# Kernel tuning notes

Measured on AMD Instinct MI355X. Metric: run time of the kernel, lower is better.

Reference implementation:

```python
import jax, jax.numpy as jnp
import numpy as np

N_HEAD = 16
THETA = 10000.0


def _rope_cos_sin(T, head_dim):
    # freqs: (T, head_dim//2), matches torch.polar(ones, outer(t, 1/theta^(2i/d)))
    inv = 1.0 / (THETA ** (jnp.arange(0, head_dim, 2, dtype=jnp.float32) / head_dim))
    freqs = jnp.arange(T, dtype=jnp.float32)[:, None] * inv[None, :]
    # broadcast shape (1, T, 1, head_dim//2) over (B, T, H, head_dim//2)
    return jnp.cos(freqs)[None, :, None, :], jnp.sin(freqs)[None, :, None, :]


def _apply_rope(t, cos, sin):
    # t: (B, T, H, hd); pairs (even, odd) form complex numbers
    B, T, H, hd = t.shape
    tr = t.astype(jnp.float32).reshape(B, T, H, hd // 2, 2)
    re, im = tr[..., 0], tr[..., 1]
    out = jnp.stack([re * cos - im * sin, re * sin + im * cos], axis=-1)
    return out.reshape(B, T, H, hd).astype(t.dtype)


def setup_inputs() -> dict:
    key = jax.random.key(0)
    k1, k2, k3 = jax.random.split(key, 3)
    C = 1024
    x = jax.random.normal(k1, (4, 2048, C), dtype=jnp.float32)
    w_attn = jax.random.normal(k2, (3 * C, C), dtype=jnp.float32) * 0.02
    w_proj = jax.random.normal(k3, (C, C), dtype=jnp.float32) * 0.02
    return {"x": x, "w_attn": w_attn, "w_proj": w_proj}


def reference(x, w_attn, w_proj):
    B, T, C = x.shape
    H = N_HEAD
    hd = C // H
    qkv = x @ w_attn.T  # (B, T, 3C) fused QKV projection
    q, k, v = jnp.split(qkv, 3, axis=-1)
    q = q.reshape(B, T, H, hd)
    k = k.reshape(B, T, H, hd)
    v = v.reshape(B, T, H, hd).transpose(0, 2, 1, 3)  # (B, H, T, hd)
    cos, sin = _rope_cos_sin(T, hd)
    q = _apply_rope(q, cos, sin).transpose(0, 2, 1, 3)  # (B, H, T, hd)
    k = _apply_rope(k, cos, sin).transpose(0, 2, 1, 3)
    scale = 1.0 / jnp.sqrt(jnp.float32(hd))
    scores = jnp.einsum('bhqd,bhkd->bhqk', q, k) * scale
    attn = jax.nn.softmax(scores, axis=-1)
    y = jnp.einsum('bhqk,bhkd->bhqd', attn, v)  # (B, H, T, hd)
    y = y.transpose(0, 2, 1, 3).reshape(B, T, C)
    return y @ w_proj.T
```

## Files before the change

### kernel.cpp

```cpp
#include <hip/hip_runtime.h>
#include <math.h>

#define BATCH 4
#define TSEQ 2048
#define CDIM 1024
#define NHEAD 16
#define HDIM 64
#define M_ROWS (BATCH * TSEQ)

typedef float f32x4 __attribute__((ext_vector_type(4)));
typedef __bf16 bf16x8 __attribute__((ext_vector_type(8)));
typedef unsigned int u32x4 __attribute__((ext_vector_type(4)));

typedef const __attribute__((address_space(1))) void gas_void;
typedef __attribute__((address_space(3))) void las_void;

static __device__ __forceinline__ unsigned short f2bf(float f) {
    unsigned int x = __float_as_uint(f);
    x += 0x7fffu + ((x >> 16) & 1u);
    return (unsigned short)(x >> 16);
}

__global__ void prep_kernel(const float* __restrict__ x, unsigned short* __restrict__ xb,
                            const float* __restrict__ wa, unsigned short* __restrict__ wab,
                            const float* __restrict__ wp, unsigned short* __restrict__ wpb,
                            float* __restrict__ cosT, float* __restrict__ sinT) {
    int blk = blockIdx.x;
    if (blk < 6144) {
        const float* in;
        unsigned short* out;
        int base;
        if (blk < 4096)      { in = x;  out = xb;  base = blk; }
        else if (blk < 5632) { in = wa; out = wab; base = blk - 4096; }
        else                 { in = wp; out = wpb; base = blk - 5632; }
        int i = (base * 256 + threadIdx.x) << 3;
        float4 a = *(const float4*)(in + i);
        float4 b = *(const float4*)(in + i + 4);
        union { unsigned short u[8]; u32x4 v; } pk;
        pk.u[0] = f2bf(a.x); pk.u[1] = f2bf(a.y); pk.u[2] = f2bf(a.z); pk.u[3] = f2bf(a.w);
        pk.u[4] = f2bf(b.x); pk.u[5] = f2bf(b.y); pk.u[6] = f2bf(b.z); pk.u[7] = f2bf(b.w);
        *(u32x4*)(out + i) = pk.v;
    } else {
        int idx = (blk - 6144) * 256 + threadIdx.x;
        int t = idx >> 5;
        int i = idx & 31;
        double inv = pow(10000.0, -((double)(2 * i)) / (double)HDIM);
        double ph = (double)t * inv;
        cosT[idx] = (float)cos(ph);
        sinT[idx] = (float)sin(ph);
    }
}

#define GROW(p) (((p) & 64) + (((p) & 15) << 2) + (((p) >> 4) & 3))
#define GEMM_CORE(A_, B_, K_, bm_, bn_)                                          \
    const int tid = threadIdx.x;                                                 \
    const int w = tid >> 6, lane = tid & 63;                                     \
    const int l15 = lane & 15, quad = lane >> 4;                                 \
    const int wm = w >> 1, wn = w & 1;                                           \
    const int srow = (w << 5) + (lane >> 2);                                     \
    const int kpart = (lane & 3) << 3;                                           \
    const unsigned short* Ag0 = A_ + (size_t)(bm_ + srow) * K_ + kpart;          \
    const unsigned short* Ag1 = A_ + (size_t)(bm_ + srow + 16) * K_ + kpart;     \
    const unsigned short* Bg0 = B_ + (size_t)(bn_ + GROW(srow)) * K_ + kpart;    \
    const unsigned short* Bg1 = B_ + (size_t)(bn_ + GROW(srow + 16)) * K_ + kpart; \
    unsigned short* Al0 = As + srow * 32 + kpart;                                \
    unsigned short* Al1 = As + (srow + 16) * 32 + kpart;                         \
    unsigned short* Bl0 = Bs + srow * 32 + kpart;                                \
    unsigned short* Bl1 = Bs + (srow + 16) * 32 + kpart;                         \
    f32x4 acc[4][4];                                                             \
    _Pragma("unroll")                                                            \
    for (int i = 0; i < 4; ++i)                                                  \
        _Pragma("unroll")                                                        \
        for (int j = 0; j < 4; ++j) acc[i][j] = (f32x4){0.f, 0.f, 0.f, 0.f};     \
    for (int k0 = 0; k0 < K_; k0 += 32) {                                        \
        __builtin_amdgcn_global_load_lds((gas_void*)(Ag0 + k0), (las_void*)Al0, 16, 0, 0); \
        __builtin_amdgcn_global_load_lds((gas_void*)(Ag1 + k0), (las_void*)Al1, 16, 0, 0); \
        __builtin_amdgcn_global_load_lds((gas_void*)(Bg0 + k0), (las_void*)Bl0, 16, 0, 0); \
        __builtin_amdgcn_global_load_lds((gas_void*)(Bg1 + k0), (las_void*)Bl1, 16, 0, 0); \
        __syncthreads();                                                         \
        bf16x8 af[4], bf[4];                                                     \
        _Pragma("unroll")                                                        \
        for (int mi = 0; mi < 4; ++mi)                                           \
            af[mi] = __builtin_bit_cast(bf16x8,                                  \
                *(const u32x4*)(As + ((wm << 6) + (mi << 4) + l15) * 32 + (quad << 3))); \
        _Pragma("unroll")                                                        \
        for (int ni = 0; ni < 4; ++ni)                                           \
            bf[ni] = __builtin_bit_cast(bf16x8,                                  \
                *(const u32x4*)(Bs + ((wn << 6) + (ni << 4) + l15) * 32 + (quad << 3))); \
        _Pragma("unroll")                                                        \
        for (int mi = 0; mi < 4; ++mi)                                           \
            _Pragma("unroll")                                                    \
            for (int ni = 0; ni < 4; ++ni)                                       \
                acc[mi][ni] = __builtin_amdgcn_mfma_f32_16x16x32_bf16(af[mi], bf[ni], acc[mi][ni], 0, 0, 0); \
        __syncthreads();                                                         \
    }

__global__ __launch_bounds__(256) void gemm_qkv_fused(
        const unsigned short* __restrict__ A, const unsigned short* __restrict__ B,
        unsigned short* __restrict__ qb, unsigned short* __restrict__ kb,
        unsigned short* __restrict__ vb,
        const float* __restrict__ cosT, const float* __restrict__ sinT) {
    __shared__ __align__(16) unsigned short As[128 * 32];
    __shared__ __align__(16) unsigned short Bs[128 * 32];
    const int bm = blockIdx.y << 7;
    const int bn = blockIdx.x << 7;
    GEMM_CORE(A, B, CDIM, bm, bn)

    const int nbase = bn + (wn << 6);
    const int mbase = bm + (wm << 6);
    const int b = mbase >> 11;
    const int tt0 = mbase & (TSEQ - 1);
    const int d0 = l15 << 2;
    const int fi = l15 << 1;

    if (nbase < 2 * CDIM) {
        const int isQ = (nbase < CDIM) ? 1 : 0;
        unsigned short* dst = isQ ? qb : kb;
        const float qs = isQ ? 0.18033688f : 1.0f;
        const int h = (nbase & (CDIM - 1)) >> 6;
        unsigned short* hb = dst + (size_t)(b * NHEAD + h) * TSEQ * HDIM;
#pragma unroll
        for (int mi = 0; mi < 4; ++mi) {
#pragma unroll
            for (int r = 0; r < 4; ++r) {
                const int t = tt0 + (mi << 4) + (quad << 2) + r;
                float2 cc = *(const float2*)(cosT + (t << 5) + fi);
                float2 ss = *(const float2*)(sinT + (t << 5) + fi);
                float re0 = acc[mi][0][r], im0 = acc[mi][1][r];
                float re1 = acc[mi][2][r], im1 = acc[mi][3][r];
                union { unsigned short u[4]; uint2 v; } pk;
                pk.u[0] = f2bf((re0 * cc.x - im0 * ss.x) * qs);
                pk.u[1] = f2bf((re0 * ss.x + im0 * cc.x) * qs);
                pk.u[2] = f2bf((re1 * cc.y - im1 * ss.y) * qs);
                pk.u[3] = f2bf((re1 * ss.y + im1 * cc.y) * qs);
                *(uint2*)(hb + (size_t)t * HDIM + d0) = pk.v;
            }
        }
    } else {
        const int h = (nbase - 2 * CDIM) >> 6;
        unsigned short* hb = vb + (size_t)(b * NHEAD + h) * HDIM * TSEQ;
#pragma unroll
        for (int mi = 0; mi < 4; ++mi) {
            const int t0 = tt0 + (mi << 4) + (quad << 2);
#pragma unroll
            for (int ni = 0; ni < 4; ++ni) {
                const int d = d0 + ni;
                union { unsigned short u[4]; uint2 v; } pk;
#pragma unroll
                for (int r = 0; r < 4; ++r) pk.u[r] = f2bf(acc[mi][ni][r]);
                *(uint2*)(hb + (size_t)d * TSEQ + t0) = pk.v;
            }
        }
    }
}

__global__ __launch_bounds__(256) void gemm_proj(
        const unsigned short* __restrict__ A, const unsigned short* __restrict__ B,
        float* __restrict__ C) {
    __shared__ __align__(16) unsigned short As[128 * 32];
    __shared__ __align__(16) unsigned short Bs[128 * 32];
    const int bm = blockIdx.y << 7;
    const int bn = blockIdx.x << 7;
    GEMM_CORE(A, B, CDIM, bm, bn)

#pragma unroll
    for (int mi = 0; mi < 4; ++mi)
#pragma unroll
        for (int r = 0; r < 4; ++r) {
            const int row = bm + (wm << 6) + (mi << 4) + (quad << 2) + r;
            float4 v = make_float4(acc[mi][0][r], acc[mi][1][r], acc[mi][2][r], acc[mi][3][r]);
            *(float4*)(C + (size_t)row * CDIM + bn + (wn << 6) + (l15 << 2)) = v;
        }
}

#define KTILE 64
#define NKT (TSEQ / KTILE)
#define QBLK 256
#define SWZ(row, ch) (((row) << 6) + ((((ch) ^ ((row) & 7))) << 3))
__global__ __launch_bounds__(256, 2) void attn_mfma(
        const unsigned short* __restrict__ qb, const unsigned short* __restrict__ kb,
        const unsigned short* __restrict__ vb, unsigned short* __restrict__ y) {
    const int bh = blockIdx.x;
    const int qt = blockIdx.y;
    const int b = bh >> 4, h = bh & 15;
    const int tid  = threadIdx.x;
    const int w    = tid >> 6;
    const int lane = tid & 63;
    const int l15  = lane & 15;
    const int quad = lane >> 4;

    __shared__ __align__(16) unsigned short Ks[2][KTILE * 64];
    __shared__ __align__(16) unsigned short Vs[2][HDIM * 64];
    __shared__ __align__(16) unsigned short Ps[4][64 * 64];

    const size_t qoff = ((size_t)bh * TSEQ + qt * QBLK + w * 64) * HDIM;
    bf16x8 aq[4][2];
#pragma unroll
    for (int mt = 0; mt < 4; ++mt)
#pragma unroll
        for (int kc2 = 0; kc2 < 2; ++kc2) {
            u32x4 v = *(const u32x4*)(qb + qoff + (size_t)(mt * 16 + l15) * HDIM + kc2 * 32 + quad * 8);
            aq[mt][kc2] = __builtin_bit_cast(bf16x8, v);
        }

    f32x4 o[4][4];
    float l_r[4][4];
#pragma unroll
    for (int mt = 0; mt < 4; ++mt)
#pragma unroll
        for (int nc = 0; nc < 4; ++nc) o[mt][nc] = (f32x4){0.f, 0.f, 0.f, 0.f};
#pragma unroll
    for (int mt = 0; mt < 4; ++mt)
#pragma unroll
        for (int r = 0; r < 4; ++r) l_r[mt][r] = 0.f;

    const unsigned short* kbase = kb + (size_t)bh * TSEQ * HDIM;
    const unsigned short* vbase = vb + (size_t)bh * HDIM * TSEQ;

    const int sr = tid >> 3;
    const int sp = (tid & 7) << 3;
    const int pp0 = ((sr & 3) << 4) + (sr >> 2);
    const int st0 = SWZ(pp0, tid & 7);
    const int st1 = SWZ(pp0 + 8, tid & 7);

    u32x4 kr[2], vr[2];
#pragma unroll
    for (int l = 0; l < 2; ++l) {
        int idx = sr + (l << 5);
        kr[l] = *(const u32x4*)(kbase + (size_t)idx * HDIM + sp);
        vr[l] = *(const u32x4*)(vbase + (size_t)idx * TSEQ + sp);
    }
    *(u32x4*)&Ks[0][st0] = kr[0];
    *(u32x4*)&Ks[0][st1] = kr[1];
    *(u32x4*)&Vs[0][st0] = vr[0];
    *(u32x4*)&Vs[0][st1] = vr[1];
#pragma unroll
    for (int l = 0; l < 2; ++l) {
        int idx = sr + (l << 5);
        kr[l] = *(const u32x4*)(kbase + (size_t)(KTILE + idx) * HDIM + sp);
        vr[l] = *(const u32x4*)(vbase + (size_t)idx * TSEQ + KTILE + sp);
    }

    for (int kt = 0; kt < NKT; ++kt) {
        const int cur = kt & 1;
        __syncthreads();

        f32x4 s[4][4];
        __builtin_amdgcn_s_setprio(1);
#pragma unroll
        for (int nc = 0; nc < 4; ++nc) {
            const int rowK = nc * 16 + l15;
            u32x4 k0 = *(const u32x4*)&Ks[cur][SWZ(rowK, quad)];
            u32x4 k1 = *(const u32x4*)&Ks[cur][SWZ(rowK, quad ^ 4)];
            bf16x8 bk0 = __builtin_bit_cast(bf16x8, k0);
            bf16x8 bk1 = __builtin_bit_cast(bf16x8, k1);
#pragma unroll
            for (int mt = 0; mt < 4; ++mt) {
                f32x4 a2 = (f32x4){0.f, 0.f, 0.f, 0.f};
                a2 = __builtin_amdgcn_mfma_f32_16x16x32_bf16(aq[mt][0], bk0, a2, 0, 0, 0);
                a2 = __builtin_amdgcn_mfma_f32_16x16x32_bf16(aq[mt][1], bk1, a2, 0, 0, 0);
                s[mt][nc] = a2;
            }
        }
        __builtin_amdgcn_s_setprio(0);

        if (kt + 1 < NKT) {
            const int nxt = cur ^ 1;
            *(u32x4*)&Ks[nxt][st0] = kr[0];
            *(u32x4*)&Ks[nxt][st1] = kr[1];
            *(u32x4*)&Vs[nxt][st0] = vr[0];
            *(u32x4*)&Vs[nxt][st1] = vr[1];
            if (kt + 2 < NKT) {
                int base = (kt + 2) * KTILE;
#pragma unroll
                for (int l = 0; l < 2; ++l) {
                    int idx = sr + (l << 5);
                    kr[l] = *(const u32x4*)(kbase + (size_t)(base + idx) * HDIM + sp);
                    vr[l] = *(const u32x4*)(vbase + (size_t)idx * TSEQ + base + sp);
                }
            }
        }

#pragma unroll
        for (int mt = 0; mt < 4; ++mt)
#pragma unroll
            for (int r = 0; r < 4; ++r) {
                float p0 = __builtin_amdgcn_exp2f(s[mt][0][r]);
                float p1 = __builtin_amdgcn_exp2f(s[mt][1][r]);
                float p2 = __builtin_amdgcn_exp2f(s[mt][2][r]);
                float p3 = __builtin_amdgcn_exp2f(s[mt][3][r]);
                l_r[mt][r] += (p0 + p1) + (p2 + p3);
                uint2 pk;
                pk.x = __builtin_amdgcn_perm(__float_as_uint(p1), __float_as_uint(p0), 0x07060302u);
                pk.y = __builtin_amdgcn_perm(__float_as_uint(p3), __float_as_uint(p2), 0x07060302u);
                const int rowP = mt * 16 + quad * 4 + r;
                *(uint2*)&Ps[w][SWZ(rowP, l15 >> 1) + ((l15 & 1) << 2)] = pk;
            }
        __threadfence_block();

        bf16x8 ap[4][2];
#pragma unroll
        for (int mt = 0; mt < 4; ++mt)
#pragma unroll
            for (int kc2 = 0; kc2 < 2; ++kc2) {
                const int rowP = mt * 16 + l15;
                u32x4 v = *(const u32x4*)&Ps[w][SWZ(rowP, kc2 * 4 + quad)];
                ap[mt][kc2] = __builtin_bit_cast(bf16x8, v);
            }
        __builtin_amdgcn_s_setprio(1);
#pragma unroll
        for (int nc = 0; nc < 4; ++nc) {
            const int rowV = nc * 16 + l15;
            u32x4 v0 = *(const u32x4*)&Vs[cur][SWZ(rowV, quad)];
            u32x4 v1 = *(const u32x4*)&Vs[cur][SWZ(rowV, quad ^ 4)];
            bf16x8 bv0 = __builtin_bit_cast(bf16x8, v0);
            bf16x8 bv1 = __builtin_bit_cast(bf16x8, v1);
#pragma unroll
            for (int mt = 0; mt < 4; ++mt) {
                o[mt][nc] = __builtin_amdgcn_mfma_f32_16x16x32_bf16(ap[mt][0], bv0, o[mt][nc], 0, 0, 0);
                o[mt][nc] = __builtin_amdgcn_mfma_f32_16x16x32_bf16(ap[mt][1], bv1, o[mt][nc], 0, 0, 0);
            }
        }
        __builtin_amdgcn_s_setprio(0);
    }

#pragma unroll
    for (int off = 1; off < 16; off <<= 1)
#pragma unroll
        for (int mt = 0; mt < 4; ++mt)
#pragma unroll
            for (int r = 0; r < 4; ++r)
                l_r[mt][r] += __shfl_xor(l_r[mt][r], off, 64);

#pragma unroll
    for (int mt = 0; mt < 4; ++mt)
#pragma unroll
        for (int r = 0; r < 4; ++r) {
            float inv_l = 1.f / l_r[mt][r];
            int t = qt * QBLK + w * 64 + mt * 16 + quad * 4 + r;
            unsigned short* row = y + (size_t)(b * TSEQ + t) * CDIM + h * HDIM;
            union { unsigned short u[4]; uint2 v; } pk;
#pragma unroll
            for (int nc = 0; nc < 4; ++nc) pk.u[nc] = f2bf(o[mt][nc][r] * inv_l);
            *(uint2*)(row + (l15 << 2)) = pk.v;
        }
}

extern "C" void kernel_launch(void* const* d_in, const int* in_sizes, int n_in,
                              void* d_out, int out_size, void* d_ws, size_t ws_size,
                              hipStream_t stream) {
    const float* x      = (const float*)d_in[0];
    const float* w_attn = (const float*)d_in[1];
    const float* w_proj = (const float*)d_in[2];
    float* out = (float*)d_out;

    unsigned short* xb  = (unsigned short*)d_ws;
    unsigned short* wab = xb  + (size_t)M_ROWS * CDIM;
    unsigned short* wpb = wab + (size_t)3 * CDIM * CDIM;
    unsigned short* qb  = wpb + (size_t)CDIM * CDIM;
    unsigned short* kb  = qb  + (size_t)BATCH * NHEAD * TSEQ * HDIM;
    unsigned short* vb  = kb  + (size_t)BATCH * NHEAD * TSEQ * HDIM;
    unsigned short* yb  = vb  + (size_t)BATCH * NHEAD * TSEQ * HDIM;
    float* cosT = (float*)(yb + (size_t)M_ROWS * CDIM);
    float* sinT = cosT + TSEQ * (HDIM / 2);

    prep_kernel<<<6400, 256, 0, stream>>>(x, xb, w_attn, wab, w_proj, wpb, cosT, sinT);

    dim3 g1(3 * CDIM / 128, M_ROWS / 128);
    gemm_qkv_fused<<<g1, 256, 0, stream>>>(xb, wab, qb, kb, vb, cosT, sinT);

    dim3 g2(BATCH * NHEAD, TSEQ / QBLK);
    attn_mfma<<<g2, 256, 0, stream>>>(qb, kb, vb, yb);

    dim3 g3(CDIM / 128, M_ROWS / 128);
    gemm_proj<<<g3, 256, 0, stream>>>(yb, wpb, out);
}
```

Before: 276.6 us.

## Compute S transposed so P stays in registers as MFMA operand, drop P LDS

The QK^T MFMA now takes swapped operands (K as A, Q as B), which yields S^T. The register layout of the exponentiated scores then matches the A-operand layout needed for the PV MFMA directly. This removes the per-warp Ps shared-memory round trip, the fence and the LDS reads, and frees 32 KB of LDS. In exchange, the V tile is stored to LDS with a new permuted layout using split 8-byte writes so the PV reduction order matches. The row-sum reduction also changes to a cross-quad shuffle plus a broadcast.

```diff
diff --git a/kernel.cpp b/kernel.cpp
--- a/kernel.cpp
+++ b/kernel.cpp
@@ -191,37 +191,43 @@
 
     __shared__ __align__(16) unsigned short Ks[2][KTILE * 64];
     __shared__ __align__(16) unsigned short Vs[2][HDIM * 64];
-    __shared__ __align__(16) unsigned short Ps[4][64 * 64];
 
     const size_t qoff = ((size_t)bh * TSEQ + qt * QBLK + w * 64) * HDIM;
     bf16x8 aq[4][2];
 #pragma unroll
-    for (int mt = 0; mt < 4; ++mt)
-#pragma unroll
-        for (int kc2 = 0; kc2 < 2; ++kc2) {
-            u32x4 v = *(const u32x4*)(qb + qoff + (size_t)(mt * 16 + l15) * HDIM + kc2 * 32 + quad * 8);
-            aq[mt][kc2] = __builtin_bit_cast(bf16x8, v);
+    for (int ni = 0; ni < 4; ++ni)
+#pragma unroll
+        for (int kc = 0; kc < 2; ++kc) {
+            u32x4 v = *(const u32x4*)(qb + qoff + (size_t)(ni * 16 + l15) * HDIM + kc * 32 + quad * 8);
+            aq[ni][kc] = __builtin_bit_cast(bf16x8, v);
         }
 
     f32x4 o[4][4];
-    float l_r[4][4];
-#pragma unroll
-    for (int mt = 0; mt < 4; ++mt)
-#pragma unroll
-        for (int nc = 0; nc < 4; ++nc) o[mt][nc] = (f32x4){0.f, 0.f, 0.f, 0.f};
-#pragma unroll
-    for (int mt = 0; mt < 4; ++mt)
-#pragma unroll
-        for (int r = 0; r < 4; ++r) l_r[mt][r] = 0.f;
+    float l_r[4];
+#pragma unroll
+    for (int ni = 0; ni < 4; ++ni) {
+        l_r[ni] = 0.f;
+#pragma unroll
+        for (int nc = 0; nc < 4; ++nc) o[ni][nc] = (f32x4){0.f, 0.f, 0.f, 0.f};
+    }
 
     const unsigned short* kbase = kb + (size_t)bh * TSEQ * HDIM;
     const unsigned short* vbase = vb + (size_t)bh * HDIM * TSEQ;
 
     const int sr = tid >> 3;
-    const int sp = (tid & 7) << 3;
-    const int pp0 = ((sr & 3) << 4) + (sr >> 2);
-    const int st0 = SWZ(pp0, tid & 7);
-    const int st1 = SWZ(pp0 + 8, tid & 7);
+    const int s8 = tid & 7;
+    const int sp = s8 << 3;
+    const int stK0 = SWZ(sr, s8);
+    const int stK1 = SWZ(sr + 32, s8);
+    const int vrow0 = ((sr & 3) << 4) + (sr >> 2);
+    const int vrow1 = vrow0 + 8;
+    const int chV  = ((s8 >> 2) << 2) + ((s8 & 1) << 1);
+    const int offV = ((s8 >> 1) & 1) << 2;
+    const int e0 = vrow0 & 7;
+    const int stV00 = (vrow0 << 6) + ((chV ^ e0) << 3) + offV;
+    const int stV01 = (vrow0 << 6) + (((chV + 1) ^ e0) << 3) + offV;
+    const int stV10 = (vrow1 << 6) + ((chV ^ e0) << 3) + offV;
+    const int stV11 = (vrow1 << 6) + (((chV + 1) ^ e0) << 3) + offV;
 
     u32x4 kr[2], vr[2];
 #pragma unroll
@@ -230,10 +236,12 @@
         kr[l] = *(const u32x4*)(kbase + (size_t)idx * HDIM + sp);
         vr[l] = *(const u32x4*)(vbase + (size_t)idx * TSEQ + sp);
     }
-    *(u32x4*)&Ks[0][st0] = kr[0];
-    *(u32x4*)&Ks[0][st1] = kr[1];
-    *(u32x4*)&Vs[0][st0] = vr[0];
-    *(u32x4*)&Vs[0][st1] = vr[1];
+    *(u32x4*)&Ks[0][stK0] = kr[0];
+    *(u32x4*)&Ks[0][stK1] = kr[1];
+    *(uint2*)&Vs[0][stV00] = make_uint2(vr[0][0], vr[0][1]);
+    *(uint2*)&Vs[0][stV01] = make_uint2(vr[0][2], vr[0][3]);
+    *(uint2*)&Vs[0][stV10] = make_uint2(vr[1][0], vr[1][1]);
+    *(uint2*)&Vs[0][stV11] = make_uint2(vr[1][2], vr[1][3]);
 #pragma unroll
     for (int l = 0; l < 2; ++l) {
         int idx = sr + (l << 5);
@@ -245,31 +253,50 @@
         const int cur = kt & 1;
         __syncthreads();
 
-        f32x4 s[4][4];
-        __builtin_amdgcn_s_setprio(1);
-#pragma unroll
-        for (int nc = 0; nc < 4; ++nc) {
-            const int rowK = nc * 16 + l15;
-            u32x4 k0 = *(const u32x4*)&Ks[cur][SWZ(rowK, quad)];
-            u32x4 k1 = *(const u32x4*)&Ks[cur][SWZ(rowK, quad ^ 4)];
-            bf16x8 bk0 = __builtin_bit_cast(bf16x8, k0);
-            bf16x8 bk1 = __builtin_bit_cast(bf16x8, k1);
-#pragma unroll
-            for (int mt = 0; mt < 4; ++mt) {
-                f32x4 a2 = (f32x4){0.f, 0.f, 0.f, 0.f};
-                a2 = __builtin_amdgcn_mfma_f32_16x16x32_bf16(aq[mt][0], bk0, a2, 0, 0, 0);
-                a2 = __builtin_amdgcn_mfma_f32_16x16x32_bf16(aq[mt][1], bk1, a2, 0, 0, 0);
-                s[mt][nc] = a2;
-            }
-        }
-        __builtin_amdgcn_s_setprio(0);
+        bf16x8 ap[4][2];
+#pragma unroll
+        for (int pvk = 0; pvk < 2; ++pvk) {
+            f32x4 s[2][4];
+#pragma unroll
+            for (int mi2 = 0; mi2 < 2; ++mi2) {
+                const int rowK = (pvk * 2 + mi2) * 16 + l15;
+                bf16x8 k0 = __builtin_bit_cast(bf16x8, *(const u32x4*)&Ks[cur][SWZ(rowK, quad)]);
+                bf16x8 k1 = __builtin_bit_cast(bf16x8, *(const u32x4*)&Ks[cur][SWZ(rowK, quad ^ 4)]);
+#pragma unroll
+                for (int ni = 0; ni < 4; ++ni) {
+                    f32x4 a2 = (f32x4){0.f, 0.f, 0.f, 0.f};
+                    a2 = __builtin_amdgcn_mfma_f32_16x16x32_bf16(k0, aq[ni][0], a2, 0, 0, 0);
+                    a2 = __builtin_amdgcn_mfma_f32_16x16x32_bf16(k1, aq[ni][1], a2, 0, 0, 0);
+                    s[mi2][ni] = a2;
+                }
+            }
+#pragma unroll
+            for (int ni = 0; ni < 4; ++ni) {
+                float p0[4], p1[4];
+#pragma unroll
+                for (int r = 0; r < 4; ++r) {
+                    p0[r] = __builtin_amdgcn_exp2f(s[0][ni][r]);
+                    p1[r] = __builtin_amdgcn_exp2f(s[1][ni][r]);
+                }
+                l_r[ni] += ((p0[0] + p0[1]) + (p0[2] + p0[3]))
+                         + ((p1[0] + p1[1]) + (p1[2] + p1[3]));
+                u32x4 pk;
+                pk[0] = __builtin_amdgcn_perm(__float_as_uint(p0[1]), __float_as_uint(p0[0]), 0x07060302u);
+                pk[1] = __builtin_amdgcn_perm(__float_as_uint(p0[3]), __float_as_uint(p0[2]), 0x07060302u);
+                pk[2] = __builtin_amdgcn_perm(__float_as_uint(p1[1]), __float_as_uint(p1[0]), 0x07060302u);
+                pk[3] = __builtin_amdgcn_perm(__float_as_uint(p1[3]), __float_as_uint(p1[2]), 0x07060302u);
+                ap[ni][pvk] = __builtin_bit_cast(bf16x8, pk);
+            }
+        }
 
         if (kt + 1 < NKT) {
             const int nxt = cur ^ 1;
-            *(u32x4*)&Ks[nxt][st0] = kr[0];
-            *(u32x4*)&Ks[nxt][st1] = kr[1];
-            *(u32x4*)&Vs[nxt][st0] = vr[0];
-            *(u32x4*)&Vs[nxt][st1] = vr[1];
+            *(u32x4*)&Ks[nxt][stK0] = kr[0];
+            *(u32x4*)&Ks[nxt][stK1] = kr[1];
+            *(uint2*)&Vs[nxt][stV00] = make_uint2(vr[0][0], vr[0][1]);
+            *(uint2*)&Vs[nxt][stV01] = make_uint2(vr[0][2], vr[0][3]);
+            *(uint2*)&Vs[nxt][stV10] = make_uint2(vr[1][0], vr[1][1]);
+            *(uint2*)&Vs[nxt][stV11] = make_uint2(vr[1][2], vr[1][3]);
             if (kt + 2 < NKT) {
                 int base = (kt + 2) * KTILE;
 #pragma unroll
@@ -282,66 +309,35 @@
         }
 
 #pragma unroll
-        for (int mt = 0; mt < 4; ++mt)
-#pragma unroll
-            for (int r = 0; r < 4; ++r) {
-                float p0 = __builtin_amdgcn_exp2f(s[mt][0][r]);
-                float p1 = __builtin_amdgcn_exp2f(s[mt][1][r]);
-                float p2 = __builtin_amdgcn_exp2f(s[mt][2][r]);
-                float p3 = __builtin_amdgcn_exp2f(s[mt][3][r]);
-                l_r[mt][r] += (p0 + p1) + (p2 + p3);
-                uint2 pk;
-                pk.x = __builtin_amdgcn_perm(__float_as_uint(p1), __float_as_uint(p0), 0x07060302u);
-                pk.y = __builtin_amdgcn_perm(__float_as_uint(p3), __float_as_uint(p2), 0x07060302u);
-                const int rowP = mt * 16 + quad * 4 + r;
-                *(uint2*)&Ps[w][SWZ(rowP, l15 >> 1) + ((l15 & 1) << 2)] = pk;
-            }
-        __threadfence_block();
-
-        bf16x8 ap[4][2];
-#pragma unroll
-        for (int mt = 0; mt < 4; ++mt)
-#pragma unroll
-            for (int kc2 = 0; kc2 < 2; ++kc2) {
-                const int rowP = mt * 16 + l15;
-                u32x4 v = *(const u32x4*)&Ps[w][SWZ(rowP, kc2 * 4 + quad)];
-                ap[mt][kc2] = __builtin_bit_cast(bf16x8, v);
-            }
-        __builtin_amdgcn_s_setprio(1);
-#pragma unroll
         for (int nc = 0; nc < 4; ++nc) {
             const int rowV = nc * 16 + l15;
-            u32x4 v0 = *(const u32x4*)&Vs[cur][SWZ(rowV, quad)];
-            u32x4 v1 = *(const u32x4*)&Vs[cur][SWZ(rowV, quad ^ 4)];
-            bf16x8 bv0 = __builtin_bit_cast(bf16x8, v0);
-            bf16x8 bv1 = __builtin_bit_cast(bf16x8, v1);
-#pragma unroll
-            for (int mt = 0; mt < 4; ++mt) {
-                o[mt][nc] = __builtin_amdgcn_mfma_f32_16x16x32_bf16(ap[mt][0], bv0, o[mt][nc], 0, 0, 0);
-                o[mt][nc] = __builtin_amdgcn_mfma_f32_16x16x32_bf16(ap[mt][1], bv1, o[mt][nc], 0, 0, 0);
-            }
-        }
-        __builtin_amdgcn_s_setprio(0);
-    }
-
-#pragma unroll
-    for (int off = 1; off < 16; off <<= 1)
-#pragma unroll
-        for (int mt = 0; mt < 4; ++mt)
-#pragma unroll
-            for (int r = 0; r < 4; ++r)
-                l_r[mt][r] += __shfl_xor(l_r[mt][r], off, 64);
-
-#pragma unroll
-    for (int mt = 0; mt < 4; ++mt)
+#pragma unroll
+            for (int kc = 0; kc < 2; ++kc) {
+                bf16x8 bv = __builtin_bit_cast(bf16x8,
+                    *(const u32x4*)&Vs[cur][SWZ(rowV, (kc << 2) + quad)]);
+#pragma unroll
+                for (int ni = 0; ni < 4; ++ni)
+                    o[ni][nc] = __builtin_amdgcn_mfma_f32_16x16x32_bf16(ap[ni][kc], bv, o[ni][nc], 0, 0, 0);
+            }
+        }
+    }
+
+#pragma unroll
+    for (int ni = 0; ni < 4; ++ni) {
+        l_r[ni] += __shfl_xor(l_r[ni], 16, 64);
+        l_r[ni] += __shfl_xor(l_r[ni], 32, 64);
+    }
+    const int srcl = (quad << 4) + (quad << 2);
+#pragma unroll
+    for (int ni = 0; ni < 4; ++ni)
 #pragma unroll
         for (int r = 0; r < 4; ++r) {
-            float inv_l = 1.f / l_r[mt][r];
-            int t = qt * QBLK + w * 64 + mt * 16 + quad * 4 + r;
+            float inv_l = 1.f / __shfl(l_r[ni], srcl + r, 64);
+            int t = qt * QBLK + w * 64 + ni * 16 + quad * 4 + r;
             unsigned short* row = y + (size_t)(b * TSEQ + t) * CDIM + h * HDIM;
             union { unsigned short u[4]; uint2 v; } pk;
 #pragma unroll
-            for (int nc = 0; nc < 4; ++nc) pk.u[nc] = f2bf(o[mt][nc][r] * inv_l);
+            for (int nc = 0; nc < 4; ++nc) pk.u[nc] = f2bf(o[ni][nc][r] * inv_l);
             *(uint2*)(row + (l15 << 2)) = pk.v;
         }
 }
```

Result: faster. 260.9 us (-5.6%).
